# Kernel optimization log

Measured on AMD Instinct MI355X. Metric: run time of the kernel, lower is better.

Reference implementation:

```python
import jax, jax.numpy as jnp
import numpy as np

B = 262144      # points per batch
DIM = 3         # input_dim
L = 16          # levels
T = 19          # log2 hash table size
F = 2           # features per level
N_MIN, N_MAX = 16, 512

_b = np.exp((np.log(N_MAX) - np.log(N_MIN)) / (L - 1))
RES = np.floor(N_MIN * _b ** np.arange(L)).astype(np.float32).reshape(1, 1, L, 1)

# voxel corner offsets [1, DIM, 1, 2^DIM]
_border = np.empty((DIM, 2 ** DIM), dtype=np.uint32)
for i in range(DIM):
    _border[i, :] = np.array(([0] * 2 ** i + [1] * 2 ** i) * 2 ** (DIM - i - 1), dtype=np.uint32)
BORDER = _border.reshape(1, DIM, 1, 2 ** DIM)

# tiny-cuda-nn hash primes; all fit in uint32. Since the torch code takes the
# result mod 2^T (a power of two), int64 and uint32 arithmetic agree on the
# low bits, so uint32 hashing is bit-exact with the original.
PRIMES = np.array([1, 2654435761, 805459861], dtype=np.uint32)
MASK = np.uint32(2 ** T - 1)


def setup_inputs() -> dict:
    key = jax.random.key(0)
    k1, k2 = jax.random.split(key)
    x = jax.random.uniform(k1, (B, DIM), dtype=jnp.float32)  # coords in [0,1)
    tables = jax.random.uniform(k2, (L, 2 ** T, F), dtype=jnp.float32,
                                minval=-1e-4, maxval=1e-4)
    return {"x": x, "tables": tables}


def reference(x, tables):
    res = jnp.asarray(RES)                                   # [1,1,L,1]
    border = jnp.asarray(BORDER)                             # [1,DIM,1,2^DIM]
    primes = jnp.asarray(PRIMES)
    scaled = x[:, :, None, None] * res                       # [B,DIM,L,1]
    grid = jnp.floor(scaled).astype(jnp.uint32) + border     # [B,DIM,L,2^DIM]
    # spatial hash: xor of per-dim coord * prime, mod 2^T
    h = (grid[:, 0] * primes[0]) ^ (grid[:, 1] * primes[1]) ^ (grid[:, 2] * primes[2])
    idx = (h & MASK).astype(jnp.int32)                       # [B,L,2^DIM]
    gathered = tables[jnp.arange(L)[None, :, None], idx]     # [B,L,2^DIM,F]
    # multilinear interpolation weights
    w = jnp.prod(1.0 - jnp.abs(scaled - grid.astype(scaled.dtype)), axis=1)  # [B,L,2^DIM]
    out = jnp.einsum('blv,blvf->blf', w, gathered)           # [B,L,F]
    return out.reshape(x.shape[0], L * F)
```

## Files before the change

### kernel.cpp

```cpp
#include <hip/hip_runtime.h>


#define NB 262144
#define NL 16
#define TSIZE (1u << 19)
#define TMASK ((1u << 19) - 1u)
#define P1 2654435761u
#define P2 805459861u

typedef float vf2 __attribute__((ext_vector_type(2)));
typedef float vf4 __attribute__((ext_vector_type(4)));

__constant__ float RES_C[NL] = {16.f, 20.f, 25.f, 32.f, 40.f, 50.f, 64.f, 80.f,
                                101.f, 128.f, 161.f, 203.f, 256.f, 322.f, 406.f, 512.f};

__device__ __forceinline__ void ngp_point_level(
    float px, float py, float pz, int l, const float* __restrict__ tables,
    float& o0, float& o1) {
  const float res = RES_C[l];
  const float sx = px * res, sy = py * res, sz = pz * res;
  const float fx = floorf(sx), fy = floorf(sy), fz = floorf(sz);
  const unsigned ix = (unsigned)fx, iy = (unsigned)fy, iz = (unsigned)fz;

  const unsigned hx0 = ix, hx1 = ix + 1u;
  const unsigned hy0 = iy * P1, hy1 = hy0 + P1;
  const unsigned hz0 = iz * P2, hz1 = hz0 + P2;

  const float wx0 = 1.0f - fabsf(sx - fx);
  const float wx1 = 1.0f - fabsf(sx - (fx + 1.0f));
  const float wy0 = 1.0f - fabsf(sy - fy);
  const float wy1 = 1.0f - fabsf(sy - (fy + 1.0f));
  const float wz0 = 1.0f - fabsf(sz - fz);
  const float wz1 = 1.0f - fabsf(sz - (fz + 1.0f));

  const vf2* __restrict__ tbl = (const vf2*)tables + (size_t)l * TSIZE;

  unsigned idxs[8];
#pragma unroll
  for (int v = 0; v < 8; ++v) {
    const unsigned hx = (v & 1) ? hx1 : hx0;
    const unsigned hy = (v & 2) ? hy1 : hy0;
    const unsigned hz = (v & 4) ? hz1 : hz0;
    idxs[v] = (hx ^ hy ^ hz) & TMASK;
  }
  vf2 g[8];
#pragma unroll
  for (int v = 0; v < 8; ++v) g[v] = tbl[idxs[v]];

  o0 = 0.0f; o1 = 0.0f;
#pragma unroll
  for (int v = 0; v < 8; ++v) {
    const float w = ((v & 1) ? wx1 : wx0) * ((v & 2) ? wy1 : wy0) * ((v & 4) ? wz1 : wz0);
    o0 = fmaf(w, g[v].x, o0);
    o1 = fmaf(w, g[v].y, o1);
  }
}

__global__ __launch_bounds__(256) void ngp_gather_kernel(
    const float* __restrict__ x,
    const float* __restrict__ tables,
    vf2* __restrict__ ws) {
  const int i = blockIdx.x;
  const int lvl = (i & 7) | ((i >> 13) << 3);
  const int chunk = (i >> 3) & 1023;
  const int b = chunk * 256 + threadIdx.x;

  const float px = __builtin_nontemporal_load(x + b * 3 + 0);
  const float py = __builtin_nontemporal_load(x + b * 3 + 1);
  const float pz = __builtin_nontemporal_load(x + b * 3 + 2);

  float o0, o1;
  ngp_point_level(px, py, pz, lvl, tables, o0, o1);

  vf2 r; r.x = o0; r.y = o1;
  __builtin_nontemporal_store(r, ws + (size_t)lvl * NB + b);
}

__global__ __launch_bounds__(256) void ngp_transpose_kernel(
    const vf2* __restrict__ ws,
    vf4* __restrict__ out4) {
  __shared__ vf2 tile[NL][257];
  const int t = threadIdx.x;
  const int p0 = blockIdx.x * 256;

#pragma unroll
  for (int l = 0; l < NL; ++l) {
    tile[l][t] = __builtin_nontemporal_load(ws + (size_t)l * NB + p0 + t);
  }
  __syncthreads();

#pragma unroll
  for (int k = 0; k < 8; ++k) {
    const int q = k * 256 + t;
    const int pq = q >> 3;
    const int wq = q & 7;
    const vf2 a = tile[2 * wq + 0][pq];
    const vf2 c = tile[2 * wq + 1][pq];
    vf4 v; v.x = a.x; v.y = a.y; v.z = c.x; v.w = c.y;
    __builtin_nontemporal_store(v, out4 + (size_t)p0 * 8 + q);
  }
}

__global__ __launch_bounds__(256) void ngp_fused_kernel(
    const float* __restrict__ x, const float* __restrict__ tables,
    float* __restrict__ out) {
  const int tid = blockIdx.x * blockDim.x + threadIdx.x;
  const int l = tid & (NL - 1);
  const int b = tid >> 4;
  float o0, o1;
  ngp_point_level(x[b * 3], x[b * 3 + 1], x[b * 3 + 2], l, tables, o0, o1);
  float2 r = make_float2(o0, o1);
  ((float2*)out)[tid] = r;
}

extern "C" void kernel_launch(void* const* d_in, const int* in_sizes, int n_in,
                              void* d_out, int out_size, void* d_ws, size_t ws_size,
                              hipStream_t stream) {
  const float* x = (const float*)d_in[0];
  const float* tables = (const float*)d_in[1];
  float* out = (float*)d_out;

  const size_t ws_needed = (size_t)NL * NB * sizeof(vf2);
  if (ws_size >= ws_needed) {
    vf2* ws = (vf2*)d_ws;
    ngp_gather_kernel<<<NB * NL / 256, 256, 0, stream>>>(x, tables, ws);
    ngp_transpose_kernel<<<NB / 256, 256, 0, stream>>>(ws, (vf4*)out);
  } else {
    ngp_fused_kernel<<<NB * NL / 256, 256, 0, stream>>>(x, tables, out);
  }
}
```

Baseline: 200.3 us.

## Spatially bucket-sort points before hash-grid gather for cache locality

```diff
diff --git a/kernel.cpp b/kernel.cpp
--- a/kernel.cpp
+++ b/kernel.cpp
@@ -7,12 +7,20 @@
 #define TMASK ((1u << 19) - 1u)
 #define P1 2654435761u
 #define P2 805459861u
+#define NBKT 32768
 
 typedef float vf2 __attribute__((ext_vector_type(2)));
 typedef float vf4 __attribute__((ext_vector_type(4)));
 
 __constant__ float RES_C[NL] = {16.f, 20.f, 25.f, 32.f, 40.f, 50.f, 64.f, 80.f,
                                 101.f, 128.f, 161.f, 203.f, 256.f, 322.f, 406.f, 512.f};
+
+__device__ __forceinline__ int bucket_of(float px, float py, float pz) {
+  int bx = min(31, (int)(px * 32.0f));
+  int by = min(31, (int)(py * 32.0f));
+  int bz = min(31, (int)(pz * 32.0f));
+  return bx | (by << 5) | (bz << 10);
+}
 
 __device__ __forceinline__ void ngp_point_level(
     float px, float py, float pz, int l, const float* __restrict__ tables,
@@ -56,39 +64,121 @@
   }
 }
 
-__global__ __launch_bounds__(256) void ngp_gather_kernel(
-    const float* __restrict__ x,
+__global__ __launch_bounds__(256) void zero_kernel(unsigned* __restrict__ hist) {
+  hist[blockIdx.x * 256 + threadIdx.x] = 0u;
+}
+
+__global__ __launch_bounds__(256) void hist_kernel(
+    const float* __restrict__ x, unsigned* __restrict__ hist) {
+  const int b = blockIdx.x * 256 + threadIdx.x;
+  const float px = x[b * 3 + 0], py = x[b * 3 + 1], pz = x[b * 3 + 2];
+  atomicAdd(&hist[bucket_of(px, py, pz)], 1u);
+}
+
+__global__ __launch_bounds__(1024) void scan_kernel(
+    const unsigned* __restrict__ hist, unsigned* __restrict__ offs) {
+  __shared__ unsigned part[1024];
+  const int t = threadIdx.x;
+  const int base = t * 32;
+  unsigned loc[32];
+  unsigned s = 0;
+#pragma unroll
+  for (int i = 0; i < 32; ++i) { loc[i] = s; s += hist[base + i]; }
+  part[t] = s;
+  __syncthreads();
+  for (int d = 1; d < 1024; d <<= 1) {
+    unsigned v = (t >= d) ? part[t - d] : 0u;
+    __syncthreads();
+    part[t] += v;
+    __syncthreads();
+  }
+  const unsigned pre = (t == 0) ? 0u : part[t - 1];
+#pragma unroll
+  for (int i = 0; i < 32; ++i) offs[base + i] = pre + loc[i];
+}
+
+__global__ __launch_bounds__(256) void scatter_kernel(
+    const float* __restrict__ x, unsigned* __restrict__ offs,
+    vf4* __restrict__ xp) {
+  const int b = blockIdx.x * 256 + threadIdx.x;
+  const float px = x[b * 3 + 0], py = x[b * 3 + 1], pz = x[b * 3 + 2];
+  const unsigned pos = atomicAdd(&offs[bucket_of(px, py, pz)], 1u);
+  vf4 v; v.x = px; v.y = py; v.z = pz; v.w = __uint_as_float((unsigned)b);
+  xp[pos] = v;
+}
+
+__global__ __launch_bounds__(256) void ngp_gather_sorted_kernel(
+    const vf4* __restrict__ xp,
     const float* __restrict__ tables,
     vf2* __restrict__ ws) {
   const int i = blockIdx.x;
   const int lvl = (i & 7) | ((i >> 13) << 3);
   const int chunk = (i >> 3) & 1023;
+  const int p = chunk * 256 + threadIdx.x;
+
+  const vf4 v = __builtin_nontemporal_load(xp + p);
+
+  float o0, o1;
+  ngp_point_level(v.x, v.y, v.z, lvl, tables, o0, o1);
+
+  vf2 r; r.x = o0; r.y = o1;
+  __builtin_nontemporal_store(r, ws + (size_t)lvl * NB + p);
+}
+
+__global__ __launch_bounds__(256) void ngp_transpose_sorted_kernel(
+    const vf2* __restrict__ ws,
+    const vf4* __restrict__ xp,
+    vf4* __restrict__ out4) {
+  __shared__ vf2 tile[NL][257];
+  __shared__ unsigned pid[256];
+  const int t = threadIdx.x;
+  const int p0 = blockIdx.x * 256;
+
+#pragma unroll
+  for (int l = 0; l < NL; ++l) {
+    tile[l][t] = __builtin_nontemporal_load(ws + (size_t)l * NB + p0 + t);
+  }
+  pid[t] = __float_as_uint(xp[p0 + t].w);
+  __syncthreads();
+
+#pragma unroll
+  for (int k = 0; k < 8; ++k) {
+    const int q = k * 256 + t;
+    const int pq = q >> 3;
+    const int wq = q & 7;
+    const vf2 a = tile[2 * wq + 0][pq];
+    const vf2 c = tile[2 * wq + 1][pq];
+    vf4 v; v.x = a.x; v.y = a.y; v.z = c.x; v.w = c.y;
+    out4[(size_t)pid[pq] * 8 + wq] = v;
+  }
+}
+
+__global__ __launch_bounds__(256) void ngp_gather_kernel(
+    const float* __restrict__ x, const float* __restrict__ tables,
+    vf2* __restrict__ ws) {
+  const int i = blockIdx.x;
+  const int lvl = (i & 7) | ((i >> 13) << 3);
+  const int chunk = (i >> 3) & 1023;
   const int b = chunk * 256 + threadIdx.x;
-
   const float px = __builtin_nontemporal_load(x + b * 3 + 0);
   const float py = __builtin_nontemporal_load(x + b * 3 + 1);
   const float pz = __builtin_nontemporal_load(x + b * 3 + 2);
-
   float o0, o1;
   ngp_point_level(px, py, pz, lvl, tables, o0, o1);
-
   vf2 r; r.x = o0; r.y = o1;
   __builtin_nontemporal_store(r, ws + (size_t)lvl * NB + b);
 }
 
 __global__ __launch_bounds__(256) void ngp_transpose_kernel(
-    const vf2* __restrict__ ws,
-    vf4* __restrict__ out4) {
+    const vf2* __restrict__ ws, vf4* __restrict__ out4) {
   __shared__ vf2 tile[NL][257];
   const int t = threadIdx.x;
   const int p0 = blockIdx.x * 256;
-
 #pragma unroll
   for (int l = 0; l < NL; ++l) {
     tile[l][t] = __builtin_nontemporal_load(ws + (size_t)l * NB + p0 + t);
   }
   __syncthreads();
-
 #pragma unroll
   for (int k = 0; k < 8; ++k) {
     const int q = k * 256 + t;
@@ -120,8 +210,25 @@
   const float* tables = (const float*)d_in[1];
   float* out = (float*)d_out;
 
-  const size_t ws_needed = (size_t)NL * NB * sizeof(vf2);
-  if (ws_size >= ws_needed) {
+  const size_t ws2_b = (size_t)NL * NB * sizeof(vf2);
+  const size_t xp_b = (size_t)NB * sizeof(vf4);
+  const size_t hist_b = (size_t)NBKT * sizeof(unsigned);
+  const size_t sorted_need = ws2_b + xp_b + 2 * hist_b;
+
+  if (ws_size >= sorted_need) {
+    char* base = (char*)d_ws;
+    vf2* ws2 = (vf2*)base;
+    vf4* xp = (vf4*)(base + ws2_b);
+    unsigned* hist = (unsigned*)(base + ws2_b + xp_b);
+    unsigned* offs = (unsigned*)(base + ws2_b + xp_b + hist_b);
+
+    zero_kernel<<<NBKT / 256, 256, 0, stream>>>(hist);
+    hist_kernel<<<NB / 256, 256, 0, stream>>>(x, hist);
+    scan_kernel<<<1, 1024, 0, stream>>>(hist, offs);
+    scatter_kernel<<<NB / 256, 256, 0, stream>>>(x, offs, xp);
+    ngp_gather_sorted_kernel<<<NB * NL / 256, 256, 0, stream>>>(xp, tables, ws2);
+    ngp_transpose_sorted_kernel<<<NB / 256, 256, 0, stream>>>(ws2, xp, (vf4*)out);
+  } else if (ws_size >= ws2_b) {
     vf2* ws = (vf2*)d_ws;
     ngp_gather_kernel<<<NB * NL / 256, 256, 0, stream>>>(x, tables, ws);
     ngp_transpose_kernel<<<NB / 256, 256, 0, stream>>>(ws, (vf4*)out);
```

Measured after the change: 214.7 us. +7.2%, slower.
